# Kernel optimization log

Measured on AMD Instinct MI355X. Metric: run time of the kernel, lower is better.

Reference implementation:

```python
import jax, jax.numpy as jnp
import numpy as np

N = 4096          # nodes
IN_F = 256        # in_features (divisible by 4)
OUT_F = 64        # out_features per head
HEADS = 4
ALPHA = 0.2       # LeakyReLU negative slope
NEG_INF = -9e15   # same masking constant as the torch code


def make_quaternion_mul(kernel):
    """kernel: [IN_F//4, OUT_F] -> hamilton: [IN_F, OUT_F].
    Mirrors the torch make_quaternion_mul (split along dim=1 into r,i,j,k)."""
    r, i, j, k = jnp.split(kernel, 4, axis=1)
    r2 = jnp.concatenate([r, -i, -j, -k], axis=1)
    i2 = jnp.concatenate([i,  r, -k,  j], axis=1)
    j2 = jnp.concatenate([j,  k,  r, -i], axis=1)
    k2 = jnp.concatenate([k, -j,  i,  r], axis=1)
    return jnp.concatenate([r2, i2, j2, k2], axis=0)


def setup_inputs() -> dict:
    key = jax.random.key(0)
    k1, k2, k3, k4 = jax.random.split(key, 4)
    x = jax.random.normal(k1, (N, IN_F), dtype=jnp.float32)
    # Glorot-ish init for quaternion kernels: [H, IN_F//4, OUT_F]
    stdv = np.sqrt(6.0 / (IN_F // 4 + OUT_F)).astype(np.float32)
    W_heads = jax.random.uniform(k2, (HEADS, IN_F // 4, OUT_F), dtype=jnp.float32,
                                 minval=-stdv, maxval=stdv)
    a_heads = jax.random.normal(k3, (HEADS, 2 * OUT_F), dtype=jnp.float32) * 0.1
    adj = (jax.random.uniform(k4, (N, N)) < 0.005).astype(jnp.float32)
    adj = jnp.maximum(adj, jnp.eye(N, dtype=jnp.float32))
    return {"x": x, "adj": adj, "W_heads": W_heads, "a_heads": a_heads}


def reference(x, adj, W_heads, a_heads):
    mask = adj > 0  # [N, N]

    def head(Wk, ak):
        hamilton = make_quaternion_mul(Wk)                # [IN_F, OUT_F]
        h = x @ hamilton                                  # [N, OUT_F]
        # e[i,j] = leakyrelu(h_i . a[:F] + h_j . a[F:]) -- equivalent to the
        # repeat/concat construction without materializing [N*N, 2F].
        e_src = h @ ak[:OUT_F]                            # [N]
        e_dst = h @ ak[OUT_F:]                            # [N]
        e = jax.nn.leaky_relu(e_src[:, None] + e_dst[None, :], negative_slope=ALPHA)
        att = jax.nn.softmax(jnp.where(mask, e, NEG_INF), axis=1)  # [N, N]
        return att @ h                                    # [N, OUT_F]

    outs = jax.vmap(head)(W_heads, a_heads)               # [H, N, OUT_F]
    out = jnp.transpose(outs, (1, 0, 2)).reshape(N, HEADS * OUT_F)
    return jax.nn.elu(out)  # concat=True path
```

## Files before the change

kernel.cpp:

```cpp
#include <hip/hip_runtime.h>

#define N 4096
#define IN_F 256
#define OUT_F 64
#define HEADS 4
#define ALPHA 0.2f
#define SEG 64

typedef __attribute__((ext_vector_type(8))) short short8;
typedef __attribute__((ext_vector_type(4))) float f32x4;

__device__ __forceinline__ unsigned short f2bf(float f) {
    unsigned u = __builtin_bit_cast(unsigned, f);
    u += 0x7fffu + ((u >> 16) & 1u);
    return (unsigned short)(u >> 16);
}

__global__ __launch_bounds__(256) void k_prep(const float* __restrict__ x,
                                              const float* __restrict__ W,
                                              unsigned short* __restrict__ xb,
                                              unsigned short* __restrict__ hamT) {
    const int tid = blockIdx.x * 256 + threadIdx.x;
    const float4 xv = *reinterpret_cast<const float4*>(x + (size_t)tid * 4);
    ushort4 o;
    o.x = f2bf(xv.x); o.y = f2bf(xv.y); o.z = f2bf(xv.z); o.w = f2bf(xv.w);
    *reinterpret_cast<ushort4*>(xb + (size_t)tid * 4) = o;

    if (tid < HEADS * OUT_F * IN_F) {
        const int hd = tid >> 14, f = (tid >> 8) & 63, k = tid & 255;
        const int q = k >> 6, kr = k & 63, p = f >> 4, fr = f & 15;
        const int   comp_t[4][4] = {{0,1,2,3},{1,0,3,2},{2,3,0,1},{3,2,1,0}};
        const float sign_t[4][4] = {{1.f,-1.f,-1.f,-1.f},
                                    {1.f, 1.f,-1.f, 1.f},
                                    {1.f, 1.f, 1.f,-1.f},
                                    {1.f,-1.f, 1.f, 1.f}};
        hamT[tid] = f2bf(sign_t[q][p] * W[(hd * 64 + kr) * 64 + comp_t[q][p] * 16 + fr]);
    }
}

__global__ __launch_bounds__(256) void k_h(const unsigned short* __restrict__ xb,
                                           const unsigned short* __restrict__ hamT,
                                           const float* __restrict__ a,
                                           float* __restrict__ h,
                                           float* __restrict__ e_src_p,
                                           float* __restrict__ e_dst_p,
                                           float* __restrict__ wmax) {
    const int wave = threadIdx.x >> 6, lane = threadIdx.x & 63;
    const int gw = blockIdx.x * 4 + wave;
    const int rg = gw >> 2, hd = gw & 3;
    const int m0 = rg * 16;
    const int r16 = lane & 15, g = lane >> 4;

    const unsigned short* xrow = xb + (size_t)(m0 + r16) * IN_F + g * 8;
    short8 af[8];
#pragma unroll
    for (int kk = 0; kk < 8; ++kk)
        af[kk] = *reinterpret_cast<const short8*>(xrow + kk * 32);

    f32x4 acc[4];
#pragma unroll
    for (int t = 0; t < 4; ++t) acc[t] = (f32x4){0.f, 0.f, 0.f, 0.f};

    const unsigned short* hbase = hamT + (size_t)(hd * 64 + r16) * IN_F + g * 8;
#pragma unroll
    for (int kk = 0; kk < 8; ++kk) {
#pragma unroll
        for (int t = 0; t < 4; ++t) {
            const short8 bf = *reinterpret_cast<const short8*>(hbase + t * 16 * IN_F + kk * 32);
            acc[t] = __builtin_amdgcn_mfma_f32_16x16x32_bf16(af[kk], bf, acc[t], 0, 0, 0);
        }
    }

    float p[4] = {0.f, 0.f, 0.f, 0.f}, q[4] = {0.f, 0.f, 0.f, 0.f};
#pragma unroll
    for (int t = 0; t < 4; ++t) {
        const float as = a[hd * 128 + t * 16 + r16];
        const float ad = a[hd * 128 + 64 + t * 16 + r16];
#pragma unroll
        for (int j = 0; j < 4; ++j) {
            const float v = acc[t][j];
            h[(size_t)(m0 + g * 4 + j) * (HEADS * OUT_F) + hd * 64 + t * 16 + r16] = v;
            p[j] = fmaf(v, as, p[j]);
            q[j] = fmaf(v, ad, q[j]);
        }
    }
#pragma unroll
    for (int off = 1; off < 16; off <<= 1) {
#pragma unroll
        for (int j = 0; j < 4; ++j) {
            p[j] += __shfl_xor(p[j], off);
            q[j] += __shfl_xor(q[j], off);
        }
    }
    if (r16 == 0) {
#pragma unroll
        for (int j = 0; j < 4; ++j) {
            e_src_p[(m0 + g * 4 + j) * 4 + hd] = p[j];
            e_dst_p[(m0 + g * 4 + j) * 4 + hd] = q[j];
        }
    }
    float qm = fmaxf(fmaxf(q[0], q[1]), fmaxf(q[2], q[3]));
    qm = fmaxf(qm, __shfl_xor(qm, 16));
    qm = fmaxf(qm, __shfl_xor(qm, 32));
    if (lane == 0) wmax[rg * 4 + hd] = qm;
}

__global__ __launch_bounds__(256) void k_dmax(const float* __restrict__ wmax,
                                              float* __restrict__ Dmax) {
    __shared__ float sm[256];
    const int hd = blockIdx.x;
    sm[threadIdx.x] = wmax[threadIdx.x * 4 + hd];
    __syncthreads();
    for (int s = 128; s > 0; s >>= 1) {
        if (threadIdx.x < s) sm[threadIdx.x] = fmaxf(sm[threadIdx.x], sm[threadIdx.x + s]);
        __syncthreads();
    }
    if (threadIdx.x == 0) Dmax[hd] = sm[0];
}

__global__ __launch_bounds__(256) void k_attn(const float* __restrict__ adj,
                                              const float* __restrict__ h,
                                              const float* __restrict__ e_src_p,
                                              const float* __restrict__ e_dst_p,
                                              const float* __restrict__ Dmax,
                                              float* __restrict__ out) {
    __shared__ int s_seg[4][SEG];
    __shared__ int s_cnt[4];
    __shared__ int s_all[4 * SEG];

    const int wave = threadIdx.x >> 6;
    const int lane = threadIdx.x & 63;
    const int i = blockIdx.x;

    const uint4* arow = reinterpret_cast<const uint4*>(adj + (size_t)i * N) + wave * 256;
    uint4 av[4];
#pragma unroll
    for (int c = 0; c < 4; ++c) av[c] = arow[c * 64 + lane];

    const unsigned long long lmask_lt = (lane == 63) ? ~0ull >> 1
                                                     : (1ull << lane) - 1ull;
    int base = 0;
#pragma unroll
    for (int c = 0; c < 4; ++c) {
#pragma unroll
        for (int s = 0; s < 4; ++s) {
            const unsigned v = (s == 0) ? av[c].x : (s == 1) ? av[c].y
                             : (s == 2) ? av[c].z : av[c].w;
            const bool hit = v != 0u;
            const unsigned long long mk = __ballot(hit);
            if (hit) {
                const int pos = base + __popcll(mk & lmask_lt);
                if (pos < SEG)
                    s_seg[wave][pos] = wave * 1024 + c * 256 + lane * 4 + s;
            }
            base += __popcll(mk);
        }
    }
    if (lane == 0) s_cnt[wave] = base < SEG ? base : SEG;
    __syncthreads();

    const int c0 = s_cnt[0], c1 = s_cnt[1], c2 = s_cnt[2], c3 = s_cnt[3];
    const int wbase = (wave > 0 ? c0 : 0) + (wave > 1 ? c1 : 0) + (wave > 2 ? c2 : 0);
    const int wcnt = s_cnt[wave];
    if (lane < wcnt) s_all[wbase + lane] = s_seg[wave][lane];
    __syncthreads();
    const int cnt = c0 + c1 + c2 + c3;

    const int hd = wave;
    const float es = e_src_p[i * 4 + hd];
    float mh = es + Dmax[hd];
    mh = mh > 0.f ? mh : ALPHA * mh;

    float lsum = 0.f, acc = 0.f;
    int e = 0;
    for (; e + 4 <= cnt; e += 4) {
        const int j0 = s_all[e], j1 = s_all[e + 1], j2 = s_all[e + 2], j3 = s_all[e + 3];
        const float d0 = e_dst_p[j0 * 4 + hd];
        const float d1 = e_dst_p[j1 * 4 + hd];
        const float d2 = e_dst_p[j2 * 4 + hd];
        const float d3 = e_dst_p[j3 * 4 + hd];
        const float h0 = h[(size_t)j0 * 256 + threadIdx.x];
        const float h1 = h[(size_t)j1 * 256 + threadIdx.x];
        const float h2 = h[(size_t)j2 * 256 + threadIdx.x];
        const float h3 = h[(size_t)j3 * 256 + threadIdx.x];
        float z0 = es + d0; z0 = z0 > 0.f ? z0 : ALPHA * z0;
        float z1 = es + d1; z1 = z1 > 0.f ? z1 : ALPHA * z1;
        float z2 = es + d2; z2 = z2 > 0.f ? z2 : ALPHA * z2;
        float z3 = es + d3; z3 = z3 > 0.f ? z3 : ALPHA * z3;
        const float w0 = __expf(z0 - mh);
        const float w1 = __expf(z1 - mh);
        const float w2 = __expf(z2 - mh);
        const float w3 = __expf(z3 - mh);
        lsum += w0 + w1 + w2 + w3;
        acc = fmaf(w0, h0, acc);
        acc = fmaf(w1, h1, acc);
        acc = fmaf(w2, h2, acc);
        acc = fmaf(w3, h3, acc);
    }
    for (; e < cnt; ++e) {
        const int j = s_all[e];
        const float d = e_dst_p[j * 4 + hd];
        const float hv = h[(size_t)j * 256 + threadIdx.x];
        float z = es + d; z = z > 0.f ? z : ALPHA * z;
        const float w = __expf(z - mh);
        lsum += w;
        acc = fmaf(w, hv, acc);
    }

    const float v = acc / lsum;
    out[(size_t)i * 256 + threadIdx.x] = v > 0.f ? v : __expf(v) - 1.f;
}

extern "C" void kernel_launch(void* const* d_in, const int* in_sizes, int n_in,
                              void* d_out, int out_size, void* d_ws, size_t ws_size,
                              hipStream_t stream) {
    const float* x   = (const float*)d_in[0];
    const float* adj = (const float*)d_in[1];
    const float* W   = (const float*)d_in[2];
    const float* a   = (const float*)d_in[3];
    float* out = (float*)d_out;

    float* ws      = (float*)d_ws;
    float* h       = ws;
    float* e_src_p = h + (size_t)N * 256;
    float* e_dst_p = e_src_p + N * 4;
    float* wmax    = e_dst_p + N * 4;
    float* Dmax    = wmax + 1024;
    unsigned short* xb   = (unsigned short*)(Dmax + 16);
    unsigned short* hamT = xb + (size_t)N * IN_F;

    k_prep<<<1024, 256, 0, stream>>>(x, W, xb, hamT);
    k_h<<<256, 256, 0, stream>>>(xb, hamT, a, h, e_src_p, e_dst_p, wmax);
    k_dmax<<<4, 256, 0, stream>>>(wmax, Dmax);
    k_attn<<<N, 256, 0, stream>>>(adj, h, e_src_p, e_dst_p, Dmax, out);
}
```

Baseline: 43.89 us.

## Replace global max bound with per-row softmax max and drop dmax kernel

Removes the k_dmax reduction kernel and the global per-head max bound. Instead, each attention row computes its logits once into shared memory, takes a wave-level max, and reuses the stored logits in the accumulation loop. The h projection kernel now splits each head's 64 output columns across two waves, doubling the grid, and writes partial e_src/e_dst values that are summed in the attention kernel. This cuts one launch and the per-edge gather of e_dst in the main loop, at the cost of an extra pass over neighbors and slightly more shared memory.

Result: faster. 42.40 us (-3.4%).

```diff
diff --git a/kernel.cpp b/kernel.cpp
--- a/kernel.cpp
+++ b/kernel.cpp
@@ -42,12 +42,13 @@
                                            const unsigned short* __restrict__ hamT,
                                            const float* __restrict__ a,
                                            float* __restrict__ h,
-                                           float* __restrict__ e_src_p,
-                                           float* __restrict__ e_dst_p,
-                                           float* __restrict__ wmax) {
+                                           float* __restrict__ esp,
+                                           float* __restrict__ edp) {
     const int wave = threadIdx.x >> 6, lane = threadIdx.x & 63;
     const int gw = blockIdx.x * 4 + wave;
-    const int rg = gw >> 2, hd = gw & 3;
+    const int rg = gw >> 3;
+    const int hd = (gw >> 1) & 3;
+    const int cf = gw & 1;
     const int m0 = rg * 16;
     const int r16 = lane & 15, g = lane >> 4;
 
@@ -57,15 +58,15 @@
     for (int kk = 0; kk < 8; ++kk)
         af[kk] = *reinterpret_cast<const short8*>(xrow + kk * 32);
 
-    f32x4 acc[4];
-#pragma unroll
-    for (int t = 0; t < 4; ++t) acc[t] = (f32x4){0.f, 0.f, 0.f, 0.f};
-
-    const unsigned short* hbase = hamT + (size_t)(hd * 64 + r16) * IN_F + g * 8;
+    f32x4 acc[2];
+#pragma unroll
+    for (int t = 0; t < 2; ++t) acc[t] = (f32x4){0.f, 0.f, 0.f, 0.f};
+
+    const unsigned short* hbase = hamT + (size_t)(hd * 64 + cf * 32 + r16) * IN_F + g * 8;
 #pragma unroll
     for (int kk = 0; kk < 8; ++kk) {
 #pragma unroll
-        for (int t = 0; t < 4; ++t) {
+        for (int t = 0; t < 2; ++t) {
             const short8 bf = *reinterpret_cast<const short8*>(hbase + t * 16 * IN_F + kk * 32);
             acc[t] = __builtin_amdgcn_mfma_f32_16x16x32_bf16(af[kk], bf, acc[t], 0, 0, 0);
         }
@@ -73,13 +74,14 @@
 
     float p[4] = {0.f, 0.f, 0.f, 0.f}, q[4] = {0.f, 0.f, 0.f, 0.f};
 #pragma unroll
-    for (int t = 0; t < 4; ++t) {
-        const float as = a[hd * 128 + t * 16 + r16];
-        const float ad = a[hd * 128 + 64 + t * 16 + r16];
+    for (int t = 0; t < 2; ++t) {
+        const int fcol = cf * 32 + t * 16 + r16;
+        const float as = a[hd * 128 + fcol];
+        const float ad = a[hd * 128 + 64 + fcol];
 #pragma unroll
         for (int j = 0; j < 4; ++j) {
             const float v = acc[t][j];
-            h[(size_t)(m0 + g * 4 + j) * (HEADS * OUT_F) + hd * 64 + t * 16 + r16] = v;
+            h[(size_t)(m0 + g * 4 + j) * (HEADS * OUT_F) + hd * 64 + fcol] = v;
             p[j] = fmaf(v, as, p[j]);
             q[j] = fmaf(v, ad, q[j]);
         }
@@ -95,38 +97,22 @@
     if (r16 == 0) {
 #pragma unroll
         for (int j = 0; j < 4; ++j) {
-            e_src_p[(m0 + g * 4 + j) * 4 + hd] = p[j];
-            e_dst_p[(m0 + g * 4 + j) * 4 + hd] = q[j];
-        }
-    }
-    float qm = fmaxf(fmaxf(q[0], q[1]), fmaxf(q[2], q[3]));
-    qm = fmaxf(qm, __shfl_xor(qm, 16));
-    qm = fmaxf(qm, __shfl_xor(qm, 32));
-    if (lane == 0) wmax[rg * 4 + hd] = qm;
-}
-
-__global__ __launch_bounds__(256) void k_dmax(const float* __restrict__ wmax,
-                                              float* __restrict__ Dmax) {
-    __shared__ float sm[256];
-    const int hd = blockIdx.x;
-    sm[threadIdx.x] = wmax[threadIdx.x * 4 + hd];
-    __syncthreads();
-    for (int s = 128; s > 0; s >>= 1) {
-        if (threadIdx.x < s) sm[threadIdx.x] = fmaxf(sm[threadIdx.x], sm[threadIdx.x + s]);
-        __syncthreads();
-    }
-    if (threadIdx.x == 0) Dmax[hd] = sm[0];
+            const int row = m0 + g * 4 + j;
+            esp[row * 8 + hd * 2 + cf] = p[j];
+            edp[row * 8 + hd * 2 + cf] = q[j];
+        }
+    }
 }
 
 __global__ __launch_bounds__(256) void k_attn(const float* __restrict__ adj,
                                               const float* __restrict__ h,
-                                              const float* __restrict__ e_src_p,
-                                              const float* __restrict__ e_dst_p,
-                                              const float* __restrict__ Dmax,
+                                              const float* __restrict__ esp,
+                                              const float* __restrict__ edp,
                                               float* __restrict__ out) {
-    __shared__ int s_seg[4][SEG];
-    __shared__ int s_cnt[4];
-    __shared__ int s_all[4 * SEG];
+    __shared__ int   s_seg[4][SEG];
+    __shared__ int   s_cnt[4];
+    __shared__ int   s_all[4 * SEG];
+    __shared__ float s_z[4][4 * SEG];
 
     const int wave = threadIdx.x >> 6;
     const int lane = threadIdx.x & 63;
@@ -167,30 +153,31 @@
     const int cnt = c0 + c1 + c2 + c3;
 
     const int hd = wave;
-    const float es = e_src_p[i * 4 + hd];
-    float mh = es + Dmax[hd];
-    mh = mh > 0.f ? mh : ALPHA * mh;
+    const float es = esp[i * 8 + hd * 2] + esp[i * 8 + hd * 2 + 1];
+    float mh = -3.0e38f;
+    for (int e = lane; e < cnt; e += 64) {
+        const int j = s_all[e];
+        const float ed = edp[j * 8 + hd * 2] + edp[j * 8 + hd * 2 + 1];
+        float z = es + ed;
+        z = z > 0.f ? z : ALPHA * z;
+        s_z[hd][e] = z;
+        mh = fmaxf(mh, z);
+    }
+#pragma unroll
+    for (int off = 32; off > 0; off >>= 1) mh = fmaxf(mh, __shfl_xor(mh, off));
 
     float lsum = 0.f, acc = 0.f;
     int e = 0;
     for (; e + 4 <= cnt; e += 4) {
         const int j0 = s_all[e], j1 = s_all[e + 1], j2 = s_all[e + 2], j3 = s_all[e + 3];
-        const float d0 = e_dst_p[j0 * 4 + hd];
-        const float d1 = e_dst_p[j1 * 4 + hd];
-        const float d2 = e_dst_p[j2 * 4 + hd];
-        const float d3 = e_dst_p[j3 * 4 + hd];
         const float h0 = h[(size_t)j0 * 256 + threadIdx.x];
         const float h1 = h[(size_t)j1 * 256 + threadIdx.x];
         const float h2 = h[(size_t)j2 * 256 + threadIdx.x];
         const float h3 = h[(size_t)j3 * 256 + threadIdx.x];
-        float z0 = es + d0; z0 = z0 > 0.f ? z0 : ALPHA * z0;
-        float z1 = es + d1; z1 = z1 > 0.f ? z1 : ALPHA * z1;
-        float z2 = es + d2; z2 = z2 > 0.f ? z2 : ALPHA * z2;
-        float z3 = es + d3; z3 = z3 > 0.f ? z3 : ALPHA * z3;
-        const float w0 = __expf(z0 - mh);
-        const float w1 = __expf(z1 - mh);
-        const float w2 = __expf(z2 - mh);
-        const float w3 = __expf(z3 - mh);
+        const float w0 = __expf(s_z[hd][e]     - mh);
+        const float w1 = __expf(s_z[hd][e + 1] - mh);
+        const float w2 = __expf(s_z[hd][e + 2] - mh);
+        const float w3 = __expf(s_z[hd][e + 3] - mh);
         lsum += w0 + w1 + w2 + w3;
         acc = fmaf(w0, h0, acc);
         acc = fmaf(w1, h1, acc);
@@ -199,10 +186,8 @@
     }
     for (; e < cnt; ++e) {
         const int j = s_all[e];
-        const float d = e_dst_p[j * 4 + hd];
         const float hv = h[(size_t)j * 256 + threadIdx.x];
-        float z = es + d; z = z > 0.f ? z : ALPHA * z;
-        const float w = __expf(z - mh);
+        const float w = __expf(s_z[hd][e] - mh);
         lsum += w;
         acc = fmaf(w, hv, acc);
     }
@@ -220,17 +205,14 @@
     const float* a   = (const float*)d_in[3];
     float* out = (float*)d_out;
 
-    float* ws      = (float*)d_ws;
-    float* h       = ws;
-    float* e_src_p = h + (size_t)N * 256;
-    float* e_dst_p = e_src_p + N * 4;
-    float* wmax    = e_dst_p + N * 4;
-    float* Dmax    = wmax + 1024;
-    unsigned short* xb   = (unsigned short*)(Dmax + 16);
+    float* ws   = (float*)d_ws;
+    float* h    = ws;
+    float* esp  = h + (size_t)N * 256;
+    float* edp  = esp + N * 8;
+    unsigned short* xb   = (unsigned short*)(edp + N * 8);
     unsigned short* hamT = xb + (size_t)N * IN_F;
 
     k_prep<<<1024, 256, 0, stream>>>(x, W, xb, hamT);
-    k_h<<<256, 256, 0, stream>>>(xb, hamT, a, h, e_src_p, e_dst_p, wmax);
-    k_dmax<<<4, 256, 0, stream>>>(wmax, Dmax);
-    k_attn<<<N, 256, 0, stream>>>(adj, h, e_src_p, e_dst_p, Dmax, out);
-}
+    k_h<<<512, 256, 0, stream>>>(xb, hamT, a, h, esp, edp);
+    k_attn<<<N, 256, 0, stream>>>(adj, h, esp, edp, out);
+}
```
